# Optimization experiments

Measured on AMD Instinct MI355X. Metric: run time of the kernel, lower is better.

## Reference

```python
import jax, jax.numpy as jnp
import numpy as np

E = 1024   # embed_dim
H = 16     # num_heads
Dh = E // H
FF = 4 * E
LN_EPS = 1e-5


def _layernorm(x, g, b):
    mu = jnp.mean(x, axis=-1, keepdims=True)
    var = jnp.var(x, axis=-1, keepdims=True)
    return (x - mu) * jax.lax.rsqrt(var + LN_EPS) * g + b


def setup_inputs() -> dict:
    key = jax.random.key(0)
    ks = jax.random.split(key, 10)
    s = lambda fan_in: 1.0 / np.sqrt(fan_in)
    x = jax.random.normal(ks[0], (2, 2048, E), dtype=jnp.float32)
    Wq = jax.random.uniform(ks[1], (H, E, Dh), jnp.float32, -s(E), s(E))
    Wk = jax.random.uniform(ks[2], (H, E, Dh), jnp.float32, -s(E), s(E))
    Wproj = jax.random.uniform(ks[3], (E, E), jnp.float32, -s(E), s(E))
    bproj = jax.random.uniform(ks[4], (E,), jnp.float32, -s(E), s(E))
    ln1_g = jnp.ones((E,), jnp.float32)
    ln1_b = jnp.zeros((E,), jnp.float32)
    ln2_g = jnp.ones((E,), jnp.float32)
    ln2_b = jnp.zeros((E,), jnp.float32)
    W1 = jax.random.uniform(ks[5], (E, FF), jnp.float32, -s(E), s(E))
    b1 = jax.random.uniform(ks[6], (FF,), jnp.float32, -s(E), s(E))
    W2 = jax.random.uniform(ks[7], (FF, E), jnp.float32, -s(FF), s(FF))
    b2 = jax.random.uniform(ks[8], (E,), jnp.float32, -s(FF), s(FF))
    return dict(x=x, Wq=Wq, Wk=Wk, Wproj=Wproj, bproj=bproj,
                ln1_g=ln1_g, ln1_b=ln1_b, ln2_g=ln2_g, ln2_b=ln2_b,
                W1=W1, b1=b1, W2=W2, b2=b2)


def reference(x, Wq, Wk, Wproj, bproj, ln1_g, ln1_b, ln2_g, ln2_b, W1, b1, W2, b2):
    B, S, _ = x.shape
    # --- self-attention branch ---
    h = _layernorm(x, ln1_g, ln1_b)
    Q = jnp.einsum('bse,hed->bhsd', h, Wq)
    K = jnp.einsum('bse,hed->bhsd', h, Wk)
    # NOTE: original code uses V = key(x), so values == keys (faithful bug).
    scores = jnp.einsum('bhqd,bhkd->bhqk', Q, K) * (1.0 / np.sqrt(Dh))
    causal = jnp.tril(jnp.ones((S, S), dtype=bool))
    scores = jnp.where(causal, scores, -jnp.inf)
    attn = jax.nn.softmax(scores, axis=-1)  # dropout is identity in eval
    out = jnp.einsum('bhqk,bhkd->bhqd', attn, K)
    out = out.transpose(0, 2, 1, 3).reshape(B, S, H * Dh)
    x = x + out @ Wproj + bproj
    # --- MLP branch ---
    h2 = _layernorm(x, ln2_g, ln2_b)
    ff = jax.nn.relu(h2 @ W1 + b1) @ W2 + b2
    return x + ff
```

## Files before the change

kernel.cpp:

```cpp
#include <hip/hip_runtime.h>
#include <stdint.h>

typedef __bf16 bf16x8 __attribute__((ext_vector_type(8)));
typedef float f32x4 __attribute__((ext_vector_type(4)));
typedef float f32x16 __attribute__((ext_vector_type(16)));
typedef unsigned short u16;
typedef unsigned int u32;

union V16 { uint4 u; u16 s[8]; bf16x8 b; };

__device__ __forceinline__ u16 f2bf(float f) {
    u32 u = __builtin_bit_cast(u32, f);
    u = (u + 0x7fffu + ((u >> 16) & 1u)) >> 16;
    return (u16)u;
}

__device__ __forceinline__ void gload16(const u16* g, u16* l) {
    __builtin_amdgcn_global_load_lds(
        (const __attribute__((address_space(1))) unsigned int*)g,
        (__attribute__((address_space(3))) unsigned int*)l,
        16, 0, 0);
}

__global__ __launch_bounds__(256)
void prep_t_kernel(const float* __restrict__ src, u16* __restrict__ dst, int R, int C) {
    __shared__ u16 tile[64 * 64];
    const int t = threadIdx.x;
    const int c0 = blockIdx.x * 64, r0 = blockIdx.y * 64;
    const size_t mbase = (size_t)blockIdx.z * R * C;
    {
        const int r = t >> 2, j4 = t & 3;
        #pragma unroll
        for (int j = 0; j < 4; ++j) {
            int c = j4 * 4 + j * 16;
            float4 v = *reinterpret_cast<const float4*>(src + mbase + (size_t)(r0 + r) * C + c0 + c);
            tile[(c + 0) * 64 + (r ^ (((c + 0) & 7) * 8))] = f2bf(v.x);
            tile[(c + 1) * 64 + (r ^ (((c + 1) & 7) * 8))] = f2bf(v.y);
            tile[(c + 2) * 64 + (r ^ (((c + 2) & 7) * 8))] = f2bf(v.z);
            tile[(c + 3) * 64 + (r ^ (((c + 3) & 7) * 8))] = f2bf(v.w);
        }
    }
    __syncthreads();
    {
        const int cc = t >> 2, j4 = t & 3;
        const int sw = (cc & 7) * 8;
        #pragma unroll
        for (int j2 = 0; j2 < 4; ++j2) {
            int rbase = j4 * 16 + j2 * 4;
            ushort4 o;
            o.x = tile[cc * 64 + ((rbase + 0) ^ sw)];
            o.y = tile[cc * 64 + ((rbase + 1) ^ sw)];
            o.z = tile[cc * 64 + ((rbase + 2) ^ sw)];
            o.w = tile[cc * 64 + ((rbase + 3) ^ sw)];
            *reinterpret_cast<ushort4*>(dst + mbase + (size_t)(c0 + cc) * R + r0 + rbase) = o;
        }
    }
}

__global__ __launch_bounds__(256)
void ln_kernel(const float* __restrict__ x, u16* __restrict__ out,
               const float* __restrict__ gw, const float* __restrict__ bw) {
    __shared__ float red[8];
    int row = blockIdx.x, t = threadIdx.x;
    float4 v = reinterpret_cast<const float4*>(x + (size_t)row * 1024)[t];
    float s = v.x + v.y + v.z + v.w;
    float sq = v.x * v.x + v.y * v.y + v.z * v.z + v.w * v.w;
    for (int o = 32; o > 0; o >>= 1) { s += __shfl_down(s, o); sq += __shfl_down(sq, o); }
    if ((t & 63) == 0) { red[t >> 6] = s; red[4 + (t >> 6)] = sq; }
    __syncthreads();
    float S  = red[0] + red[1] + red[2] + red[3];
    float SQ = red[4] + red[5] + red[6] + red[7];
    float mean = S * (1.f / 1024.f);
    float var  = SQ * (1.f / 1024.f) - mean * mean;
    float rstd = rsqrtf(var + 1e-5f);
    float4 g4 = reinterpret_cast<const float4*>(gw)[t];
    float4 b4 = reinterpret_cast<const float4*>(bw)[t];
    ushort4 o;
    o.x = f2bf((v.x - mean) * rstd * g4.x + b4.x);
    o.y = f2bf((v.y - mean) * rstd * g4.y + b4.y);
    o.z = f2bf((v.z - mean) * rstd * g4.z + b4.z);
    o.w = f2bf((v.w - mean) * rstd * g4.w + b4.w);
    reinterpret_cast<ushort4*>(out + (size_t)row * 1024)[t] = o;
}

template<int EPI, typename OT>
__global__ __launch_bounds__(256)
void gemm_bt(const u16* __restrict__ A, const u16* __restrict__ B,
             OT* __restrict__ C, const float* __restrict__ bias,
             const float* __restrict__ res, int K, int N, u16* __restrict__ ktr) {
    __shared__ u16 Al[128 * 64];
    __shared__ u16 Bl[128 * 64];
    const int t = threadIdx.x;
    const int lane = t & 63;
    const int w = t >> 6;
    const int wm = w >> 1, wn = w & 1;
    const int l15 = lane & 15, gq = lane >> 4;
    const int gx = gridDim.x;
    const int nwg = gx * gridDim.y;
    const int bid = blockIdx.y * gx + blockIdx.x;
    const int sw = ((nwg & 7) == 0) ? ((bid & 7) * (nwg >> 3) + (bid >> 3)) : bid;
    const int col0 = (sw % gx) * 128;
    const int row0 = (sw / gx) * 128;

    f32x4 acc[4][4] = {};

    const int nkb = K >> 6;
    for (int kb = 0; kb < nkb; ++kb) {
        #pragma unroll
        for (int i = 0; i < 4; ++i) {
            int slot = i * 256 + t;
            int r = slot >> 3;
            int g = (slot & 7) ^ (r & 7);
            gload16(A + (size_t)(row0 + r) * K + kb * 64 + g * 8, Al + slot * 8);
            gload16(B + (size_t)(col0 + r) * K + kb * 64 + g * 8, Bl + slot * 8);
        }
        __syncthreads();
        #pragma unroll
        for (int s = 0; s < 2; ++s) {
            bf16x8 af[4], bfr[4];
            #pragma unroll
            for (int mi = 0; mi < 4; ++mi) {
                int rl = wm * 64 + mi * 16 + l15;
                int ba = rl * 128 + ((s * 64 + gq * 16) ^ ((rl & 7) << 4));
                af[mi] = *reinterpret_cast<const bf16x8*>(reinterpret_cast<const char*>(Al) + ba);
            }
            #pragma unroll
            for (int ni = 0; ni < 4; ++ni) {
                int rl = wn * 64 + ni * 16 + l15;
                int ba = rl * 128 + ((s * 64 + gq * 16) ^ ((rl & 7) << 4));
                bfr[ni] = *reinterpret_cast<const bf16x8*>(reinterpret_cast<const char*>(Bl) + ba);
            }
            #pragma unroll
            for (int mi = 0; mi < 4; ++mi)
                #pragma unroll
                for (int ni = 0; ni < 4; ++ni)
                    acc[mi][ni] = __builtin_amdgcn_mfma_f32_16x16x32_bf16(af[mi], bfr[ni], acc[mi][ni], 0, 0, 0);
        }
        __syncthreads();
    }

    #pragma unroll
    for (int mi = 0; mi < 4; ++mi) {
        #pragma unroll
        for (int ni = 0; ni < 4; ++ni) {
            int gcol = col0 + wn * 64 + ni * 16 + l15;
            int grow0 = row0 + wm * 64 + mi * 16 + gq * 4;
            #pragma unroll
            for (int r = 0; r < 4; ++r) {
                int grow = grow0 + r;
                float v = acc[mi][ni][r];
                if constexpr (EPI == 1 || EPI == 2) v += bias[gcol];
                if constexpr (EPI == 1) v += res[(size_t)grow * N + gcol];
                if constexpr (EPI == 2) v = fmaxf(v, 0.f);
                if constexpr (sizeof(OT) == 4) C[(size_t)grow * N + gcol] = v;
                else                           C[(size_t)grow * N + gcol] = f2bf(v);
            }
        }
    }
}

#define DS_A(MH) \
  _Pragma("unroll") \
  for (int mi = 0; mi < 4; ++mi) { \
    const int rl = wm * 128 + (MH) * 64 + mi * 16 + l15; \
    const char* rp = abase + rl * 128; \
    const int sw2 = (rl & 7) << 4; \
    af[mi][0] = *reinterpret_cast<const bf16x8*>(rp + ((gq * 16) ^ sw2)); \
    af[mi][1] = *reinterpret_cast<const bf16x8*>(rp + ((64 + gq * 16) ^ sw2)); \
  }

#define DS_B(NH) \
  _Pragma("unroll") \
  for (int ni = 0; ni < 2; ++ni) { \
    const int rl = wn * 64 + (NH) * 32 + ni * 16 + l15; \
    const char* rp = bbase + rl * 128; \
    const int sw2 = (rl & 7) << 4; \
    bfr[ni][0] = *reinterpret_cast<const bf16x8*>(rp + ((gq * 16) ^ sw2)); \
    bfr[ni][1] = *reinterpret_cast<const bf16x8*>(rp + ((64 + gq * 16) ^ sw2)); \
  }

#define ST_A(HALF, KP, DB) \
  _Pragma("unroll") \
  for (int i = 0; i < 2; ++i) { \
    const int idx = i * 512 + t; const int rs = idx >> 3; const int kc = idx & 7; \
    const int row = (rs & 63) + ((rs >> 6) << 7) + (HALF) * 64; \
    gload16(Ag + (size_t)(row0 + row) * Kf + (KP) + ((kc ^ (row & 7)) << 3), (DB) + row * 64 + kc * 8); \
  }

#define ST_B(HALF, KP, DB) \
  _Pragma("unroll") \
  for (int i = 0; i < 2; ++i) { \
    const int idx = i * 512 + t; const int rs = idx >> 3; const int kc = idx & 7; \
    const int row = (rs & 31) + ((rs >> 5) << 6) + (HALF) * 32; \
    gload16(Bg + (size_t)(col0 + row) * Kf + (KP) + ((kc ^ (row & 7)) << 3), (DB) + row * 64 + kc * 8); \
  }

#define MFMA_Q(MH, NH) \
  _Pragma("unroll") \
  for (int mi = 0; mi < 4; ++mi) { \
    _Pragma("unroll") \
    for (int ni = 0; ni < 2; ++ni) { \
      acc[MH][mi][NH][ni] = __builtin_amdgcn_mfma_f32_16x16x32_bf16(af[mi][0], bfr[ni][0], acc[MH][mi][NH][ni], 0, 0, 0); \
      acc[MH][mi][NH][ni] = __builtin_amdgcn_mfma_f32_16x16x32_bf16(af[mi][1], bfr[ni][1], acc[MH][mi][NH][ni], 0, 0, 0); \
    } \
  }

#define WAITV(N) asm volatile("s_waitcnt vmcnt(" #N ")" ::: "memory")
#define BAR() __builtin_amdgcn_s_barrier()
#define PRIO1() __builtin_amdgcn_s_setprio(1)
#define PRIO0() __builtin_amdgcn_s_setprio(0)

template<int EPI, typename OT>
__global__ __launch_bounds__(512, 2)
void gemm256(const u16* __restrict__ A, const u16* __restrict__ B, OT* __restrict__ C,
             const float* __restrict__ bias, const float* __restrict__ res,
             int Kf, int KC, int N, u16* __restrict__ ktr) {
    __shared__ u16 AL[2][16384];
    __shared__ u16 BL[2][16384];
    const int t = threadIdx.x;
    const int lane = t & 63;
    const int w = t >> 6;
    const int wm = w >> 2, wn = w & 3;
    const int l15 = lane & 15, gq = lane >> 4;
    const int gx = gridDim.x;
    const int nwg = gx * gridDim.y;
    const int bid = blockIdx.y * gx + blockIdx.x;
    const int sw = ((nwg & 7) == 0) ? ((bid & 7) * (nwg >> 3) + (bid >> 3)) : bid;
    const int col0 = (sw % gx) * 256;
    const int row0 = (sw / gx) * 256;
    const int kbase = blockIdx.z * KC;
    const u16* Ag = A;
    const u16* Bg = B;

    f32x4 acc[2][4][2][2] = {};
    bf16x8 af[4][2], bfr[2][2];

    const int NT = KC >> 6;
    { u16* An = &AL[0][0]; u16* Bn = &BL[0][0];
      ST_A(0, kbase, An); ST_B(0, kbase, Bn); ST_B(1, kbase, Bn); ST_A(1, kbase, An); }
    WAITV(4);
    BAR();

    for (int tI = 0; tI < NT - 1; ++tI) {
        const int c = tI & 1;
        const char* abase = reinterpret_cast<const char*>(&AL[c][0]);
        const char* bbase = reinterpret_cast<const char*>(&BL[c][0]);
        u16* An = &AL[c ^ 1][0];
        u16* Bn = &BL[c ^ 1][0];
        const int kn = kbase + (tI + 1) * 64;
        DS_A(0); DS_B(0);
        ST_A(0, kn, An);
        WAITV(4); BAR();
        PRIO1(); MFMA_Q(0, 0); PRIO0();
        BAR();
        DS_B(1);
        ST_B(0, kn, Bn);
        WAITV(4); BAR();
        PRIO1(); MFMA_Q(0, 1); PRIO0();
        BAR();
        DS_A(1); DS_B(0);
        ST_B(1, kn, Bn);
        BAR();
        PRIO1(); MFMA_Q(1, 0); PRIO0();
        BAR();
        DS_B(1);
        ST_A(1, kn, An);
        WAITV(4); BAR();
        PRIO1(); MFMA_Q(1, 1); PRIO0();
        BAR();
    }
    {
        const int c = (NT - 1) & 1;
        const char* abase = reinterpret_cast<const char*>(&AL[c][0]);
        const char* bbase = reinterpret_cast<const char*>(&BL[c][0]);
        DS_A(0); DS_B(0);
        WAITV(2); BAR();
        PRIO1(); MFMA_Q(0, 0); PRIO0();
        BAR();
        DS_B(1);
        WAITV(0); BAR();
        PRIO1(); MFMA_Q(0, 1); PRIO0();
        BAR();
        DS_A(1); DS_B(0);
        BAR();
        PRIO1(); MFMA_Q(1, 0); PRIO0();
        BAR();
        DS_B(1);
        PRIO1(); MFMA_Q(1, 1); PRIO0();
    }

    const size_t Crow0 = (size_t)blockIdx.z * ((size_t)gridDim.y * 256);
    #pragma unroll
    for (int mh = 0; mh < 2; ++mh)
    #pragma unroll
    for (int mi = 0; mi < 4; ++mi)
    #pragma unroll
    for (int nh = 0; nh < 2; ++nh)
    #pragma unroll
    for (int ni = 0; ni < 2; ++ni) {
        const int gcol = col0 + wn * 64 + nh * 32 + ni * 16 + l15;
        const int grow0 = row0 + wm * 128 + mh * 64 + mi * 16 + gq * 4;
        f32x4 v = acc[mh][mi][nh][ni];
        if constexpr (EPI == 2) {
            const float bb = bias[gcol];
            v[0] += bb; v[1] += bb; v[2] += bb; v[3] += bb;
        }
        #pragma unroll
        for (int r = 0; r < 4; ++r) {
            const size_t o = (Crow0 + grow0 + r) * N + gcol;
            float x = v[r];
            if constexpr (EPI == 2) x = fmaxf(x, 0.f);
            if constexpr (sizeof(OT) == 4) C[o] = x;
            else                           C[o] = f2bf(x);
        }
        if constexpr (EPI == 3) {
            if (gcol >= 1024) {
                ushort4 k4;
                k4.x = f2bf(v[0]); k4.y = f2bf(v[1]); k4.z = f2bf(v[2]); k4.w = f2bf(v[3]);
                *reinterpret_cast<ushort4*>(ktr + (size_t)(gcol - 1024) * 4096 + grow0) = k4;
            }
        }
    }
}

__global__ __launch_bounds__(256)
void reduce4_kernel(const float4* __restrict__ p0, const float4* __restrict__ p1,
                    const float4* __restrict__ p2, const float4* __restrict__ p3,
                    const float4* __restrict__ xm, const float* __restrict__ b2,
                    float4* __restrict__ out) {
    const int i = blockIdx.x * 256 + threadIdx.x;
    float4 a = p0[i], b = p1[i], c = p2[i], d = p3[i], x = xm[i];
    const float4 bb = *reinterpret_cast<const float4*>(b2 + ((i & 255) << 2));
    float4 o;
    o.x = x.x + bb.x + a.x + b.x + c.x + d.x;
    o.y = x.y + bb.y + a.y + b.y + c.y + d.y;
    o.z = x.z + bb.z + a.z + b.z + c.z + d.z;
    o.w = x.w + bb.w + a.w + b.w + c.w + d.w;
    out[i] = o;
}

__global__ __launch_bounds__(256)
void attn_kernel(const u16* __restrict__ qk, const u16* __restrict__ ktr, u16* __restrict__ out) {
    __shared__ u16 Kl[2][64 * 64];
    __shared__ u16 Tl[2][64 * 64];
    const int t = threadIdx.x;
    const int lane = t & 63;
    const int w = t >> 6;
    const int l31 = lane & 31, hi = lane >> 5;
    const int flat = blockIdx.x;
    const int bh = flat & 31;
    const int tt = flat >> 5;
    const int qb = (tt < 8) ? tt : 23 - tt;
    const int b = bh >> 4, h = bh & 15;
    const int q0w = qb * 128 + w * 32;
    const int q = q0w + l31;
    const u16* Qp = qk + (size_t)b * 2048 * 2048 + h * 64;
    const u16* Kp = Qp + 1024;
    const u16* Tp = ktr + (size_t)h * 64 * 4096 + (size_t)b * 2048;

    bf16x8 qf[4];
    #pragma unroll
    for (int s = 0; s < 4; ++s)
        qf[s] = *reinterpret_cast<const bf16x8*>(Qp + (size_t)q * 2048 + s * 16 + hi * 8);

    f32x16 oacc[2] = {};
    float m_run = -3.0e38f, l_run = 0.f;
    const int qwmax = q0w + 31;
    const int nt = (qb * 128 + 128) >> 6;

    {
        #pragma unroll
        for (int i = 0; i < 2; ++i) {
            int slot = i * 256 + t;
            int r = slot >> 3;
            int g = (slot & 7) ^ (r & 7);
            gload16(Kp + (size_t)r * 2048 + g * 8, &Kl[0][0] + slot * 8);
            gload16(Tp + (size_t)r * 4096 + g * 8, &Tl[0][0] + slot * 8);
        }
    }

    for (int kt = 0; kt < nt; ++kt) {
        const int cur = kt & 1;
        __syncthreads();
        if (kt + 1 < nt) {
            int k0 = (kt + 1) * 64;
            #pragma unroll
            for (int i = 0; i < 2; ++i) {
                int slot = i * 256 + t;
                int r = slot >> 3;
                int g = (slot & 7) ^ (r & 7);
                gload16(Kp + (size_t)(k0 + r) * 2048 + g * 8, &Kl[cur ^ 1][0] + slot * 8);
                gload16(Tp + (size_t)r * 4096 + k0 + g * 8, &Tl[cur ^ 1][0] + slot * 8);
            }
        }
        const u16* kl = &Kl[cur][0];
        const u16* tl = &Tl[cur][0];
        #pragma unroll
        for (int s2 = 0; s2 < 2; ++s2) {
            const int ks = s2 * 32;
            const int kbase = kt * 64 + ks;
            if (kbase > qwmax) continue;
            f32x16 st = {};
            #pragma unroll
            for (int s = 0; s < 4; ++s) {
                int r = ks + l31;
                int col = (16 * s + 8 * hi) ^ ((r & 7) * 8);
                bf16x8 kf = *reinterpret_cast<const bf16x8*>(kl + r * 64 + col);
                st = __builtin_amdgcn_mfma_f32_32x32x16_bf16(kf, qf[s], st, 0, 0, 0);
            }
            float p[16];
            float mt = -3.0e38f;
            if (kbase + 31 <= q0w) {
                #pragma unroll
                for (int i = 0; i < 16; ++i) { p[i] = st[i] * 0.125f; mt = fmaxf(mt, p[i]); }
            } else {
                #pragma unroll
                for (int i = 0; i < 16; ++i) {
                    int kloc = (i & 3) + 8 * (i >> 2) + 4 * hi;
                    float v = st[i] * 0.125f;
                    v = (kbase + kloc <= q) ? v : -3.0e38f;
                    p[i] = v;
                    mt = fmaxf(mt, v);
                }
            }
            mt = fmaxf(mt, __shfl_xor(mt, 32));
            float mn = fmaxf(m_run, mt);
            float alpha = __expf(m_run - mn);
            float rs = 0.f;
            #pragma unroll
            for (int i = 0; i < 16; ++i) {
                float e = __expf(p[i] - mn);
                p[i] = e;
                rs += e;
            }
            rs += __shfl_xor(rs, 32);
            l_run = l_run * alpha + rs;
            m_run = mn;
            oacc[0] *= alpha;
            oacc[1] *= alpha;
            u32 wds[8], xw[8];
            #pragma unroll
            for (int j = 0; j < 8; ++j) {
                u16 a = __builtin_bit_cast(u16, (__bf16)p[2 * j]);
                u16 c = __builtin_bit_cast(u16, (__bf16)p[2 * j + 1]);
                wds[j] = (u32)a | ((u32)c << 16);
            }
            #pragma unroll
            for (int j = 0; j < 8; ++j) xw[j] = (u32)__shfl_xor((int)wds[j], 32);
            union PF { u32 wd[4]; bf16x8 b; } pf[2];
            if (hi == 0) {
                pf[0].wd[0] = wds[0]; pf[0].wd[1] = wds[1]; pf[0].wd[2] = xw[0]; pf[0].wd[3] = xw[1];
                pf[1].wd[0] = wds[4]; pf[1].wd[1] = wds[5]; pf[1].wd[2] = xw[4]; pf[1].wd[3] = xw[5];
            } else {
                pf[0].wd[0] = xw[2]; pf[0].wd[1] = xw[3]; pf[0].wd[2] = wds[2]; pf[0].wd[3] = wds[3];
                pf[1].wd[0] = xw[6]; pf[1].wd[1] = xw[7]; pf[1].wd[2] = wds[6]; pf[1].wd[3] = wds[7];
            }
            #pragma unroll
            for (int kc = 0; kc < 2; ++kc) {
                #pragma unroll
                for (int db = 0; db < 2; ++db) {
                    int r = db * 32 + l31;
                    int col = (ks + 16 * kc + 8 * hi) ^ ((r & 7) * 8);
                    bf16x8 vf = *reinterpret_cast<const bf16x8*>(tl + r * 64 + col);
                    oacc[db] = __builtin_amdgcn_mfma_f32_32x32x16_bf16(vf, pf[kc].b, oacc[db], 0, 0, 0);
                }
            }
        }
    }

    const float inv = 1.f / l_run;
    u16* op = out + (size_t)(b * 2048 + q) * 1024 + h * 64;
    #pragma unroll
    for (int db = 0; db < 2; ++db) {
        #pragma unroll
        for (int tq = 0; tq < 4; ++tq) {
            ushort4 o;
            o.x = f2bf(oacc[db][tq * 4 + 0] * inv);
            o.y = f2bf(oacc[db][tq * 4 + 1] * inv);
            o.z = f2bf(oacc[db][tq * 4 + 2] * inv);
            o.w = f2bf(oacc[db][tq * 4 + 3] * inv);
            *reinterpret_cast<ushort4*>(op + db * 32 + tq * 8 + hi * 4) = o;
        }
    }
}

extern "C" void kernel_launch(void* const* d_in, const int* in_sizes, int n_in,
                              void* d_out, int out_size, void* d_ws, size_t ws_size,
                              hipStream_t stream) {
    const float* x     = (const float*)d_in[0];
    const float* Wq    = (const float*)d_in[1];
    const float* Wk    = (const float*)d_in[2];
    const float* Wproj = (const float*)d_in[3];
    const float* bproj = (const float*)d_in[4];
    const float* ln1g  = (const float*)d_in[5];
    const float* ln1b  = (const float*)d_in[6];
    const float* ln2g  = (const float*)d_in[7];
    const float* ln2b  = (const float*)d_in[8];
    const float* W1    = (const float*)d_in[9];
    const float* b1    = (const float*)d_in[10];
    const float* W2    = (const float*)d_in[11];
    const float* b2    = (const float*)d_in[12];

    char* ws = (char*)d_ws;
    u16*   wqkT   = (u16*)(ws + 0);
    u16*   wprojT = (u16*)(ws + (4ull << 20));
    u16*   w1T    = (u16*)(ws + (6ull << 20));
    u16*   w2T    = (u16*)(ws + (14ull << 20));
    u16*   hbuf   = (u16*)(ws + (22ull << 20));
    float* xmid   = (float*)(ws + (30ull << 20));
    u16*   qk     = (u16*)(ws + (46ull << 20));
    u16*   ktr    = (u16*)(ws + (62ull << 20));
    u16*   attnb  = (u16*)(ws + (70ull << 20));
    u16*   ff     = (u16*)(ws + (46ull << 20));
    float* part   = (float*)(ws + (78ull << 20));
    const bool fastW2 = ws_size >= (142ull << 20);

    prep_t_kernel<<<dim3(1, 16, 16), 256, 0, stream>>>(Wq, wqkT, 1024, 64);
    prep_t_kernel<<<dim3(1, 16, 16), 256, 0, stream>>>(Wk, wqkT + 1024 * 1024, 1024, 64);
    prep_t_kernel<<<dim3(16, 16, 1), 256, 0, stream>>>(Wproj, wprojT, 1024, 1024);
    prep_t_kernel<<<dim3(64, 16, 1), 256, 0, stream>>>(W1, w1T, 1024, 4096);
    prep_t_kernel<<<dim3(16, 64, 1), 256, 0, stream>>>(W2, w2T, 4096, 1024);

    ln_kernel<<<4096, 256, 0, stream>>>(x, hbuf, ln1g, ln1b);
    gemm256<3, u16><<<dim3(8, 16, 1), 512, 0, stream>>>(hbuf, wqkT, qk, nullptr, nullptr, 1024, 1024, 2048, ktr);
    attn_kernel<<<512, 256, 0, stream>>>(qk, ktr, attnb);
    gemm_bt<1, float><<<dim3(8, 32), 256, 0, stream>>>(attnb, wprojT, xmid, bproj, x, 1024, 1024, nullptr);
    ln_kernel<<<4096, 256, 0, stream>>>(xmid, hbuf, ln2g, ln2b);
    gemm256<2, u16><<<dim3(16, 16, 1), 512, 0, stream>>>(hbuf, w1T, ff, b1, nullptr, 1024, 1024, 4096, nullptr);
    if (fastW2) {
        gemm256<0, float><<<dim3(4, 16, 4), 512, 0, stream>>>(ff, w2T, part, nullptr, nullptr, 4096, 1024, 1024, nullptr);
        reduce4_kernel<<<4096, 256, 0, stream>>>(
            (const float4*)part, (const float4*)(part + 4194304),
            (const float4*)(part + 2 * 4194304), (const float4*)(part + 3 * 4194304),
            (const float4*)xmid, b2, (float4*)d_out);
    } else {
        gemm_bt<1, float><<<dim3(8, 32), 256, 0, stream>>>(ff, w2T, (float*)d_out, b2, xmid, 4096, 1024, nullptr);
    }
}
```

Measured before the change: 258.6 us.

## Fold softmax scale into Q, widen attention step, split-K proj fused with LN2

Q is pre-scaled by 0.125·log2(e) in the QK GEMM epilogue so attention can use exp2f with no per-score multiply. The attention loop now handles a full 64-key tile per step with two interleaved QK MFMAs, and skips rescaling the running max unless it rises past a threshold. MFMA blocks are wrapped in priority hints. The output projection becomes a 2-way split-K gemm256 whose partials are reduced together with residual, bias and LayerNorm2 in one new kernel. The lazy-rescale threshold and bf16 probabilities bring some numerical risk, and PRIO1/PRIO0 must already be defined elsewhere.

Result: slower. 268.6 us (+3.9%).

```diff
diff --git a/kernel.cpp b/kernel.cpp
--- a/kernel.cpp
+++ b/kernel.cpp
@@ -6,8 +6,6 @@
 typedef float f32x16 __attribute__((ext_vector_type(16)));
 typedef unsigned short u16;
 typedef unsigned int u32;
-
-union V16 { uint4 u; u16 s[8]; bf16x8 b; };
 
 __device__ __forceinline__ u16 f2bf(float f) {
     u32 u = __builtin_bit_cast(u32, f);
@@ -83,6 +81,42 @@
     reinterpret_cast<ushort4*>(out + (size_t)row * 1024)[t] = o;
 }
 
+__global__ __launch_bounds__(256)
+void ln2red_kernel(const float4* __restrict__ p0, const float4* __restrict__ p1,
+                   const float4* __restrict__ x4, const float* __restrict__ bproj,
+                   const float* __restrict__ gw, const float* __restrict__ bw,
+                   float4* __restrict__ xmid, u16* __restrict__ out) {
+    __shared__ float red[8];
+    const int row = blockIdx.x, t = threadIdx.x;
+    const size_t idx = (size_t)row * 256 + t;
+    float4 a = p0[idx], b = p1[idx], xx = x4[idx];
+    const float4 bp = *reinterpret_cast<const float4*>(bproj + (t << 2));
+    float4 v;
+    v.x = a.x + b.x + xx.x + bp.x;
+    v.y = a.y + b.y + xx.y + bp.y;
+    v.z = a.z + b.z + xx.z + bp.z;
+    v.w = a.w + b.w + xx.w + bp.w;
+    xmid[idx] = v;
+    float s = v.x + v.y + v.z + v.w;
+    float sq = v.x * v.x + v.y * v.y + v.z * v.z + v.w * v.w;
+    for (int o = 32; o > 0; o >>= 1) { s += __shfl_down(s, o); sq += __shfl_down(sq, o); }
+    if ((t & 63) == 0) { red[t >> 6] = s; red[4 + (t >> 6)] = sq; }
+    __syncthreads();
+    float S  = red[0] + red[1] + red[2] + red[3];
+    float SQ = red[4] + red[5] + red[6] + red[7];
+    float mean = S * (1.f / 1024.f);
+    float var  = SQ * (1.f / 1024.f) - mean * mean;
+    float rstd = rsqrtf(var + 1e-5f);
+    const float4 g4 = *reinterpret_cast<const float4*>(gw + (t << 2));
+    const float4 b4 = *reinterpret_cast<const float4*>(bw + (t << 2));
+    ushort4 o;
+    o.x = f2bf((v.x - mean) * rstd * g4.x + b4.x);
+    o.y = f2bf((v.y - mean) * rstd * g4.y + b4.y);
+    o.z = f2bf((v.z - mean) * rstd * g4.z + b4.z);
+    o.w = f2bf((v.w - mean) * rstd * g4.w + b4.w);
+    *reinterpret_cast<ushort4*>(out + idx * 4) = o;
+}
+
 template<int EPI, typename OT>
 __global__ __launch_bounds__(256)
 void gemm_bt(const u16* __restrict__ A, const u16* __restrict__ B,
@@ -305,6 +339,12 @@
             const float bb = bias[gcol];
             v[0] += bb; v[1] += bb; v[2] += bb; v[3] += bb;
         }
+        if constexpr (EPI == 3) {
+            if (gcol < 1024) {
+                const float QS = 0.18033688f;
+                v[0] *= QS; v[1] *= QS; v[2] *= QS; v[3] *= QS;
+            }
+        }
         #pragma unroll
         for (int r = 0; r < 4; ++r) {
             const size_t o = (Crow0 + grow0 + r) * N + gcol;
@@ -393,79 +433,103 @@
                 gload16(Tp + (size_t)r * 4096 + k0 + g * 8, &Tl[cur ^ 1][0] + slot * 8);
             }
         }
+        const int kbase = kt * 64;
+        if (kbase > qwmax) continue;
         const u16* kl = &Kl[cur][0];
         const u16* tl = &Tl[cur][0];
-        #pragma unroll
-        for (int s2 = 0; s2 < 2; ++s2) {
-            const int ks = s2 * 32;
-            const int kbase = kt * 64 + ks;
-            if (kbase > qwmax) continue;
-            f32x16 st = {};
-            #pragma unroll
-            for (int s = 0; s < 4; ++s) {
-                int r = ks + l31;
+
+        f32x16 st0 = {}, st1 = {};
+        PRIO1();
+        #pragma unroll
+        for (int s = 0; s < 4; ++s) {
+            {
+                int r = l31;
                 int col = (16 * s + 8 * hi) ^ ((r & 7) * 8);
                 bf16x8 kf = *reinterpret_cast<const bf16x8*>(kl + r * 64 + col);
-                st = __builtin_amdgcn_mfma_f32_32x32x16_bf16(kf, qf[s], st, 0, 0, 0);
-            }
-            float p[16];
-            float mt = -3.0e38f;
-            if (kbase + 31 <= q0w) {
-                #pragma unroll
-                for (int i = 0; i < 16; ++i) { p[i] = st[i] * 0.125f; mt = fmaxf(mt, p[i]); }
-            } else {
-                #pragma unroll
-                for (int i = 0; i < 16; ++i) {
-                    int kloc = (i & 3) + 8 * (i >> 2) + 4 * hi;
-                    float v = st[i] * 0.125f;
-                    v = (kbase + kloc <= q) ? v : -3.0e38f;
-                    p[i] = v;
-                    mt = fmaxf(mt, v);
-                }
-            }
-            mt = fmaxf(mt, __shfl_xor(mt, 32));
-            float mn = fmaxf(m_run, mt);
-            float alpha = __expf(m_run - mn);
-            float rs = 0.f;
+                st0 = __builtin_amdgcn_mfma_f32_32x32x16_bf16(kf, qf[s], st0, 0, 0, 0);
+            }
+            {
+                int r = 32 + l31;
+                int col = (16 * s + 8 * hi) ^ ((r & 7) * 8);
+                bf16x8 kf = *reinterpret_cast<const bf16x8*>(kl + r * 64 + col);
+                st1 = __builtin_amdgcn_mfma_f32_32x32x16_bf16(kf, qf[s], st1, 0, 0, 0);
+            }
+        }
+        PRIO0();
+
+        float p[32];
+        if (kbase + 63 <= q0w) {
+            #pragma unroll
+            for (int i = 0; i < 16; ++i) { p[i] = st0[i]; p[16 + i] = st1[i]; }
+        } else {
             #pragma unroll
             for (int i = 0; i < 16; ++i) {
-                float e = __expf(p[i] - mn);
-                p[i] = e;
-                rs += e;
-            }
-            rs += __shfl_xor(rs, 32);
-            l_run = l_run * alpha + rs;
-            m_run = mn;
+                int kloc = kbase + (i & 3) + 8 * (i >> 2) + 4 * hi;
+                p[i]      = (kloc      <= q) ? st0[i] : -3.0e38f;
+                p[16 + i] = (kloc + 32 <= q) ? st1[i] : -3.0e38f;
+            }
+        }
+        float m4[8];
+        #pragma unroll
+        for (int i = 0; i < 8; ++i)
+            m4[i] = fmaxf(fmaxf(p[4 * i], p[4 * i + 1]), fmaxf(p[4 * i + 2], p[4 * i + 3]));
+        float mt = fmaxf(fmaxf(fmaxf(m4[0], m4[1]), fmaxf(m4[2], m4[3])),
+                         fmaxf(fmaxf(m4[4], m4[5]), fmaxf(m4[6], m4[7])));
+        mt = fmaxf(mt, __shfl_xor(mt, 32));
+
+        float mn = m_run;
+        if (!__all(mt <= m_run + 11.5f)) {
+            mn = fmaxf(m_run, mt);
+            float alpha = exp2f(m_run - mn);
+            l_run *= alpha;
             oacc[0] *= alpha;
             oacc[1] *= alpha;
-            u32 wds[8], xw[8];
-            #pragma unroll
-            for (int j = 0; j < 8; ++j) {
-                u16 a = __builtin_bit_cast(u16, (__bf16)p[2 * j]);
-                u16 c = __builtin_bit_cast(u16, (__bf16)p[2 * j + 1]);
-                wds[j] = (u32)a | ((u32)c << 16);
-            }
-            #pragma unroll
-            for (int j = 0; j < 8; ++j) xw[j] = (u32)__shfl_xor((int)wds[j], 32);
-            union PF { u32 wd[4]; bf16x8 b; } pf[2];
-            if (hi == 0) {
-                pf[0].wd[0] = wds[0]; pf[0].wd[1] = wds[1]; pf[0].wd[2] = xw[0]; pf[0].wd[3] = xw[1];
-                pf[1].wd[0] = wds[4]; pf[1].wd[1] = wds[5]; pf[1].wd[2] = xw[4]; pf[1].wd[3] = xw[5];
-            } else {
-                pf[0].wd[0] = xw[2]; pf[0].wd[1] = xw[3]; pf[0].wd[2] = wds[2]; pf[0].wd[3] = wds[3];
-                pf[1].wd[0] = xw[6]; pf[1].wd[1] = xw[7]; pf[1].wd[2] = wds[6]; pf[1].wd[3] = wds[7];
-            }
-            #pragma unroll
-            for (int kc = 0; kc < 2; ++kc) {
-                #pragma unroll
-                for (int db = 0; db < 2; ++db) {
-                    int r = db * 32 + l31;
-                    int col = (ks + 16 * kc + 8 * hi) ^ ((r & 7) * 8);
-                    bf16x8 vf = *reinterpret_cast<const bf16x8*>(tl + r * 64 + col);
-                    oacc[db] = __builtin_amdgcn_mfma_f32_32x32x16_bf16(vf, pf[kc].b, oacc[db], 0, 0, 0);
-                }
-            }
-        }
+            m_run = mn;
+        }
+        float s0 = 0.f, s1 = 0.f, s2 = 0.f, s3 = 0.f;
+        #pragma unroll
+        for (int i = 0; i < 32; ++i) p[i] = exp2f(p[i] - mn);
+        #pragma unroll
+        for (int i = 0; i < 8; ++i) {
+            s0 += p[4 * i]; s1 += p[4 * i + 1]; s2 += p[4 * i + 2]; s3 += p[4 * i + 3];
+        }
+        float rs = (s0 + s1) + (s2 + s3);
+        rs += __shfl_xor(rs, 32);
+        l_run += rs;
+
+        u32 wds[16], xw[16];
+        #pragma unroll
+        for (int j = 0; j < 16; ++j) {
+            u16 a = __builtin_bit_cast(u16, (__bf16)p[2 * j]);
+            u16 c = __builtin_bit_cast(u16, (__bf16)p[2 * j + 1]);
+            wds[j] = (u32)a | ((u32)c << 16);
+        }
+        #pragma unroll
+        for (int j = 0; j < 16; ++j) xw[j] = (u32)__shfl_xor((int)wds[j], 32);
+        union PF { u32 wd[4]; bf16x8 b; } pf[4];
+        if (hi == 0) {
+            pf[0].wd[0] = wds[0];  pf[0].wd[1] = wds[1];  pf[0].wd[2] = xw[0];   pf[0].wd[3] = xw[1];
+            pf[1].wd[0] = wds[4];  pf[1].wd[1] = wds[5];  pf[1].wd[2] = xw[4];   pf[1].wd[3] = xw[5];
+            pf[2].wd[0] = wds[8];  pf[2].wd[1] = wds[9];  pf[2].wd[2] = xw[8];   pf[2].wd[3] = xw[9];
+            pf[3].wd[0] = wds[12]; pf[3].wd[1] = wds[13]; pf[3].wd[2] = xw[12];  pf[3].wd[3] = xw[13];
+        } else {
+            pf[0].wd[0] = xw[2];   pf[0].wd[1] = xw[3];   pf[0].wd[2] = wds[2];  pf[0].wd[3] = wds[3];
+            pf[1].wd[0] = xw[6];   pf[1].wd[1] = xw[7];   pf[1].wd[2] = wds[6];  pf[1].wd[3] = wds[7];
+            pf[2].wd[0] = xw[10];  pf[2].wd[1] = xw[11];  pf[2].wd[2] = wds[10]; pf[2].wd[3] = wds[11];
+            pf[3].wd[0] = xw[14];  pf[3].wd[1] = xw[15];  pf[3].wd[2] = wds[14]; pf[3].wd[3] = wds[15];
+        }
+        PRIO1();
+        #pragma unroll
+        for (int kc = 0; kc < 4; ++kc) {
+            #pragma unroll
+            for (int db = 0; db < 2; ++db) {
+                int r = db * 32 + l31;
+                int col = (kc * 16 + 8 * hi) ^ ((r & 7) * 8);
+                bf16x8 vf = *reinterpret_cast<const bf16x8*>(tl + r * 64 + col);
+                oacc[db] = __builtin_amdgcn_mfma_f32_32x32x16_bf16(vf, pf[kc].b, oacc[db], 0, 0, 0);
+            }
+        }
+        PRIO0();
     }
 
     const float inv = 1.f / l_run;
@@ -513,7 +577,7 @@
     u16*   attnb  = (u16*)(ws + (70ull << 20));
     u16*   ff     = (u16*)(ws + (46ull << 20));
     float* part   = (float*)(ws + (78ull << 20));
-    const bool fastW2 = ws_size >= (142ull << 20);
+    const bool fast = ws_size >= (142ull << 20);
 
     prep_t_kernel<<<dim3(1, 16, 16), 256, 0, stream>>>(Wq, wqkT, 1024, 64);
     prep_t_kernel<<<dim3(1, 16, 16), 256, 0, stream>>>(Wk, wqkT + 1024 * 1024, 1024, 64);
@@ -524,10 +588,17 @@
     ln_kernel<<<4096, 256, 0, stream>>>(x, hbuf, ln1g, ln1b);
     gemm256<3, u16><<<dim3(8, 16, 1), 512, 0, stream>>>(hbuf, wqkT, qk, nullptr, nullptr, 1024, 1024, 2048, ktr);
     attn_kernel<<<512, 256, 0, stream>>>(qk, ktr, attnb);
-    gemm_bt<1, float><<<dim3(8, 32), 256, 0, stream>>>(attnb, wprojT, xmid, bproj, x, 1024, 1024, nullptr);
-    ln_kernel<<<4096, 256, 0, stream>>>(xmid, hbuf, ln2g, ln2b);
+    if (fast) {
+        gemm256<0, float><<<dim3(4, 16, 2), 512, 0, stream>>>(attnb, wprojT, part, nullptr, nullptr, 1024, 512, 1024, nullptr);
+        ln2red_kernel<<<4096, 256, 0, stream>>>(
+            (const float4*)part, (const float4*)(part + 4194304), (const float4*)x,
+            bproj, ln2g, ln2b, (float4*)xmid, hbuf);
+    } else {
+        gemm_bt<1, float><<<dim3(8, 32), 256, 0, stream>>>(attnb, wprojT, xmid, bproj, x, 1024, 1024, nullptr);
+        ln_kernel<<<4096, 256, 0, stream>>>(xmid, hbuf, ln2g, ln2b);
+    }
     gemm256<2, u16><<<dim3(16, 16, 1), 512, 0, stream>>>(hbuf, w1T, ff, b1, nullptr, 1024, 1024, 4096, nullptr);
-    if (fastW2) {
+    if (fast) {
         gemm256<0, float><<<dim3(4, 16, 4), 512, 0, stream>>>(ff, w2T, part, nullptr, nullptr, 4096, 1024, 1024, nullptr);
         reduce4_kernel<<<4096, 256, 0, stream>>>(
             (const float4*)part, (const float4*)(part + 4194304),
```
